# Kernel optimization log

Hardware: AMD Instinct MI355X
Metric: run time of the kernel (lower is better)

## Reference

```python
import jax, jax.numpy as jnp
import numpy as np

NSLICES = 4
HID = 512
IN_DIM = 342   # input_shape - 1 (last column is phase)
OUT_DIM = 311
BATCH = 1024


def _cubic(y0, y1, y2, y3, mu):
    mu2 = mu * mu
    mu3 = mu2 * mu
    return ((-0.5 * y0 + 1.5 * y1 - 1.5 * y2 + 0.5 * y3) * mu3
            + (y0 - 2.5 * y1 + 2.0 * y2 - 0.5 * y3) * mu2
            + (-0.5 * y0 + 0.5 * y2) * mu
            + y1)


def setup_inputs() -> dict:
    key = jax.random.key(0)
    kx, k0, k1, k2 = jax.random.split(key, 4)
    x = jax.random.uniform(kx, (BATCH, IN_DIM + 1), dtype=jnp.float32)
    W0 = jax.random.normal(k0, (NSLICES, HID, IN_DIM), dtype=jnp.float32) * 0.1
    W1 = jax.random.normal(k1, (NSLICES, HID, HID), dtype=jnp.float32) * 0.1
    W2 = jax.random.normal(k2, (NSLICES, OUT_DIM, HID), dtype=jnp.float32) * 0.1
    b0 = jnp.zeros((NSLICES, HID), dtype=jnp.float32)
    b1 = jnp.zeros((NSLICES, HID), dtype=jnp.float32)
    b2 = jnp.zeros((NSLICES, OUT_DIM), dtype=jnp.float32)
    return {"x": x, "W0": W0, "W1": W1, "W2": W2, "b0": b0, "b1": b1, "b2": b2}


def reference(x, W0, W1, W2, b0, b1, b2):
    data, phase = x[:, :-1], x[:, -1]          # [B, 342], [B]
    pscale = NSLICES * phase                    # phase in [0,1) -> pscale in [0,4)
    mu = pscale % 1.0                           # [B]
    i1 = pscale.astype(jnp.int32) % NSLICES
    i0 = (i1 - 1) % NSLICES
    i2 = (i1 + 1) % NSLICES
    i3 = (i1 + 2) % NSLICES

    muW = mu[:, None, None]
    mub = mu[:, None]

    # Per-sample interpolated weights/biases (gather 4 slices + cubic blend)
    W0i = _cubic(W0[i0], W0[i1], W0[i2], W0[i3], muW)   # [B, 512, 342]
    W1i = _cubic(W1[i0], W1[i1], W1[i2], W1[i3], muW)   # [B, 512, 512]
    W2i = _cubic(W2[i0], W2[i1], W2[i2], W2[i3], muW)   # [B, 311, 512]
    b0i = _cubic(b0[i0], b0[i1], b0[i2], b0[i3], mub)   # [B, 512]
    b1i = _cubic(b1[i0], b1[i1], b1[i2], b1[i3], mub)   # [B, 512]
    b2i = _cubic(b2[i0], b2[i1], b2[i2], b2[i3], mub)   # [B, 311]

    # 3-layer MLP with per-sample weights (batched GEMV); dropout in eval mode (identity)
    H1 = jax.nn.elu(jnp.einsum('boi,bi->bo', W0i, data) + b0i)
    H2 = jax.nn.elu(jnp.einsum('boi,bi->bo', W1i, H1) + b1i)
    H3 = jnp.einsum('boi,bi->bo', W2i, H2) + b2i
    return H3
```

## Files before the change

kernel.cpp:

```cpp
#include <hip/hip_runtime.h>
#include <hip/hip_fp16.h>
#include <math.h>

typedef _Float16 f16x8 __attribute__((ext_vector_type(8)));
typedef float f32x4 __attribute__((ext_vector_type(4)));

#define NS 4
#define HID 512
#define IN_DIM 342
#define OUT_DIM 311
#define BATCH 1024
#define INP 352
#define K0V (NS*INP)
#define K12V (NS*HID)
#define XROW (IN_DIM+1)

#define OFF_ACOEF 0
#define OFF_X0H   4096
#define OFF_W0H   (OFF_X0H + 720896)
#define OFF_W1H   (OFF_W0H + 360448)
#define OFF_W2H   (OFF_W1H + 524288)
#define OFF_H1X   (OFF_W2H + 327680)
#define OFF_H2X   OFF_X0H

typedef __attribute__((address_space(3))) void lds_t;
typedef __attribute__((address_space(1))) const void gvm_t;
__device__ __forceinline__ void gload16(const void* g, void* l) {
    __builtin_amdgcn_global_load_lds((gvm_t*)g, (lds_t*)l, 16, 0, 0);
}

__global__ __launch_bounds__(256) void prep_all(
    const float* __restrict__ x,
    const float* __restrict__ W0, const float* __restrict__ W1,
    const float* __restrict__ W2,
    float* __restrict__ acoef,
    __half* __restrict__ X0h, __half* __restrict__ W0h,
    __half* __restrict__ W1h, __half* __restrict__ W2h)
{
    const int bid = blockIdx.x;
    const int t = threadIdx.x;
    if (bid < 512) {
        int o = bid;
        if (t < 176) {
            int s = t / 44;
            int cm = t - s*44;
            int i = cm * 8;
            f16x8 h = {};
            if (i + 8 <= IN_DIM) {
                const float* src = W0 + ((size_t)s*HID + o)*IN_DIM + i;
                float4 v0 = *(const float4*)(src);
                float4 v1 = *(const float4*)(src + 4);
                h[0]=(_Float16)v0.x; h[1]=(_Float16)v0.y; h[2]=(_Float16)v0.z; h[3]=(_Float16)v0.w;
                h[4]=(_Float16)v1.x; h[5]=(_Float16)v1.y; h[6]=(_Float16)v1.z; h[7]=(_Float16)v1.w;
            } else if (i < IN_DIM) {
                const float* src = W0 + ((size_t)s*HID + o)*IN_DIM + i;
                #pragma unroll
                for (int j=0;j<8;++j) h[j] = (_Float16)((i+j < IN_DIM) ? src[j] : 0.f);
            }
            *(f16x8*)(W0h + (size_t)o*K0V + s*INP + i) = h;
        }
    } else if (bid < 1024) {
        int o = bid - 512;
        int k = t * 8;
        int s = k >> 9, i = k & 511;
        const float* src = W1 + ((size_t)s*HID + o)*HID + i;
        float4 v0 = *(const float4*)(src);
        float4 v1 = *(const float4*)(src + 4);
        f16x8 h;
        h[0]=(_Float16)v0.x; h[1]=(_Float16)v0.y; h[2]=(_Float16)v0.z; h[3]=(_Float16)v0.w;
        h[4]=(_Float16)v1.x; h[5]=(_Float16)v1.y; h[6]=(_Float16)v1.z; h[7]=(_Float16)v1.w;
        *(f16x8*)(W1h + (size_t)o*K12V + k) = h;
    } else if (bid < 1344) {
        int o = bid - 1024;
        int k = t * 8;
        int s = k >> 9, i = k & 511;
        f16x8 h = {};
        if (o < OUT_DIM) {
            const float* src = W2 + ((size_t)s*OUT_DIM + o)*HID + i;
            float4 v0 = *(const float4*)(src);
            float4 v1 = *(const float4*)(src + 4);
            h[0]=(_Float16)v0.x; h[1]=(_Float16)v0.y; h[2]=(_Float16)v0.z; h[3]=(_Float16)v0.w;
            h[4]=(_Float16)v1.x; h[5]=(_Float16)v1.y; h[6]=(_Float16)v1.z; h[7]=(_Float16)v1.w;
        }
        *(f16x8*)(W2h + (size_t)o*K12V + k) = h;
    } else {
        int b = bid - 1344;
        float phase = x[(size_t)b*XROW + IN_DIM];
        float ps = (float)NS * phase;
        float mu = ps - floorf(ps);
        int i1 = ((int)ps) & (NS-1);
        float mu2 = mu*mu, mu3 = mu2*mu;
        float r0 =  1.5f*mu3 - 2.5f*mu2 + 1.0f;
        float r1 = -1.5f*mu3 + 2.0f*mu2 + 0.5f*mu;
        float r2 =  0.5f*mu3 - 0.5f*mu2;
        float r3 = -0.5f*mu3 +      mu2 - 0.5f*mu;
        if (t < 4) {
            int rel = (t - i1) & 3;
            acoef[b*4 + t] = (rel==0)?r0:(rel==1)?r1:(rel==2)?r2:r3;
        }
        if (t < 176) {
            int s = t / 44;
            int cm = t - s*44;
            int i = cm * 8;
            int rel = (s - i1) & 3;
            float sc = (rel==0)?r0:(rel==1)?r1:(rel==2)?r2:r3;
            f16x8 h = {};
            if (i + 8 <= IN_DIM) {
                const float* src = x + (size_t)b*XROW + i;
                float4 v0 = *(const float4*)(src);
                float4 v1 = *(const float4*)(src + 4);
                h[0]=(_Float16)(v0.x*sc); h[1]=(_Float16)(v0.y*sc);
                h[2]=(_Float16)(v0.z*sc); h[3]=(_Float16)(v0.w*sc);
                h[4]=(_Float16)(v1.x*sc); h[5]=(_Float16)(v1.y*sc);
                h[6]=(_Float16)(v1.z*sc); h[7]=(_Float16)(v1.w*sc);
            } else if (i < IN_DIM) {
                const float* src = x + (size_t)b*XROW + i;
                #pragma unroll
                for (int j=0;j<8;++j) h[j] = (_Float16)((i+j < IN_DIM) ? src[j]*sc : 0.f);
            }
            *(f16x8*)(X0h + (size_t)b*K0V + s*INP + i) = h;
        }
    }
}

template<int LAYER>
__global__ __launch_bounds__(256) void gemm_mfma(
    const __half* __restrict__ A,
    const __half* __restrict__ Bw,
    const float* __restrict__ acoef,
    const float* __restrict__ bias,
    __half* __restrict__ outH,
    float* __restrict__ outF)
{
    constexpr int K  = (LAYER==0) ? K0V : K12V;
    constexpr int NB = (LAYER==2) ? OUT_DIM : HID;
    constexpr int NITER = K / 128;

    __shared__ __align__(16) char lbuf[4][24576];

    const int t    = threadIdx.x;
    const int lane = t & 63;
    const int wid  = t >> 6;
    const int wm   = wid >> 1;
    const int wn   = wid & 1;
    const int m0   = blockIdx.y * 32;
    const int n0   = blockIdx.x * 64;

    const int cS = lane & 15;
    const int r4 = lane >> 4;
    const int rA0 = 4*(wid    ) + r4;
    const int rA1 = 4*(wid + 4) + r4;
    const __half* aSrc0 = A + (size_t)(m0 + rA0)*K + (((cS&8)|((cS&7)^(rA0&7))) * 8);
    const __half* aSrc1 = A + (size_t)(m0 + rA1)*K + (((cS&8)|((cS&7)^(rA1&7))) * 8);
    const int rB0 = 4*(wid     ) + r4;
    const int rB1 = 4*(wid +  4) + r4;
    const int rB2 = 4*(wid +  8) + r4;
    const int rB3 = 4*(wid + 12) + r4;
    const __half* bSrc0 = Bw + (size_t)(n0 + rB0)*K + (((cS&8)|((cS&7)^(rB0&7))) * 8);
    const __half* bSrc1 = Bw + (size_t)(n0 + rB1)*K + (((cS&8)|((cS&7)^(rB1&7))) * 8);
    const __half* bSrc2 = Bw + (size_t)(n0 + rB2)*K + (((cS&8)|((cS&7)^(rB2&7))) * 8);
    const __half* bSrc3 = Bw + (size_t)(n0 + rB3)*K + (((cS&8)|((cS&7)^(rB3&7))) * 8);

    f32x4 acc[2] = {};

    auto stage = [&](int it) {
        char* base = lbuf[it & 3];
        const int ko = it * 128;
        gload16(aSrc0 + ko, base + (wid    )*1024);
        gload16(aSrc1 + ko, base + (wid + 4)*1024);
        gload16(bSrc0 + ko, base + 8192 + (wid     )*1024);
        gload16(bSrc1 + ko, base + 8192 + (wid +  4)*1024);
        gload16(bSrc2 + ko, base + 8192 + (wid +  8)*1024);
        gload16(bSrc3 + ko, base + 8192 + (wid + 12)*1024);
    };

    stage(0);
    stage(1);
    stage(2);

    for (int it = 0; it < NITER; ++it) {
        if (it + 2 < NITER)      asm volatile("s_waitcnt vmcnt(12)" ::: "memory");
        else if (it + 1 < NITER) asm volatile("s_waitcnt vmcnt(6)"  ::: "memory");
        else                     asm volatile("s_waitcnt vmcnt(0)"  ::: "memory");
        __builtin_amdgcn_s_barrier();
        __builtin_amdgcn_sched_barrier(0);
        if (it + 3 < NITER) stage(it + 3);
        const char* sA = lbuf[it & 3];
        const char* sB = sA + 8192;
        #pragma unroll
        for (int kk = 0; kk < 4; ++kk) {
            const int kb = kk*64 + (lane>>4)*16;
            const int rr = wm*16 + (lane&15);
            f16x8 af = *(const f16x8*)(sA + rr*256 + (kb ^ ((rr&7)<<4)));
            #pragma unroll
            for (int ni = 0; ni < 2; ++ni) {
                const int oo = wn*32 + ni*16 + (lane&15);
                f16x8 bf = *(const f16x8*)(sB + oo*256 + (kb ^ ((oo&7)<<4)));
                acc[ni] = __builtin_amdgcn_mfma_f32_16x16x32_f16(af, bf, acc[ni], 0, 0, 0);
            }
        }
    }

    #pragma unroll
    for (int r = 0; r < 4; ++r) {
        const int row = m0 + wm*16 + (lane>>4)*4 + r;
        const float c0 = acoef[row*4+0], c1 = acoef[row*4+1],
                    c2 = acoef[row*4+2], c3 = acoef[row*4+3];
        #pragma unroll
        for (int ni = 0; ni < 2; ++ni) {
            const int col = n0 + wn*32 + ni*16 + (lane&15);
            float v = acc[ni][r];
            if (LAYER == 2) {
                if (col < OUT_DIM) {
                    float bi = c0*bias[col] + c1*bias[NB+col]
                             + c2*bias[2*NB+col] + c3*bias[3*NB+col];
                    outF[(size_t)row*OUT_DIM + col] = v + bi;
                }
            } else {
                float bi = c0*bias[col] + c1*bias[NB+col]
                         + c2*bias[2*NB+col] + c3*bias[3*NB+col];
                v += bi;
                v = (v > 0.f) ? v : expm1f(v);
                size_t o = (size_t)row*K12V + col;
                outH[o        ] = __float2half(c0*v);
                outH[o +   HID] = __float2half(c1*v);
                outH[o + 2*HID] = __float2half(c2*v);
                outH[o + 3*HID] = __float2half(c3*v);
            }
        }
    }
}

extern "C" void kernel_launch(void* const* d_in, const int* in_sizes, int n_in,
                              void* d_out, int out_size, void* d_ws, size_t ws_size,
                              hipStream_t stream) {
    const float* x  = (const float*)d_in[0];
    const float* W0 = (const float*)d_in[1];
    const float* W1 = (const float*)d_in[2];
    const float* W2 = (const float*)d_in[3];
    const float* b0 = (const float*)d_in[4];
    const float* b1 = (const float*)d_in[5];
    const float* b2 = (const float*)d_in[6];
    float* out = (float*)d_out;
    float* ws  = (float*)d_ws;

    float*  acoef = ws + OFF_ACOEF;
    __half* X0h   = (__half*)(ws + OFF_X0H);
    __half* W0h   = (__half*)(ws + OFF_W0H);
    __half* W1h   = (__half*)(ws + OFF_W1H);
    __half* W2h   = (__half*)(ws + OFF_W2H);
    __half* H1x   = (__half*)(ws + OFF_H1X);
    __half* H2x   = (__half*)(ws + OFF_H2X);

    prep_all<<<dim3(2368), dim3(256), 0, stream>>>(x, W0, W1, W2, acoef,
                                                   X0h, W0h, W1h, W2h);

    gemm_mfma<0><<<dim3(HID/64, BATCH/32), dim3(256), 0, stream>>>(
        X0h, W0h, acoef, b0, H1x, nullptr);
    gemm_mfma<1><<<dim3(HID/64, BATCH/32), dim3(256), 0, stream>>>(
        H1x, W1h, acoef, b1, H2x, nullptr);
    gemm_mfma<2><<<dim3(320/64, BATCH/32), dim3(256), 0, stream>>>(
        H2x, W2h, acoef, b2, nullptr, out);
}
```

Measured before the change: 37.84 us.

## Interleave slice dimension in packed K layout for W1/W2 and hidden activations

Changes the packed fp16 K-dimension layout for layers 1 and 2 from slice-major (s*512+i) to slice-interleaved (i*4+s). The weight packing now reads float2 from all four slices, and the epilogue writes the four coefficient-scaled hidden values as one 8-byte vector store instead of four scattered 2-byte stores. It also loads the four blend coefficients with a single vector load. The aim is cheaper activation stores; the GEMM's K ordering must match consistently between weights and activations, and the weight reads become less contiguous.

Result: no change. 37.74 us (-0.3%).

```diff
diff --git a/kernel.cpp b/kernel.cpp
--- a/kernel.cpp
+++ b/kernel.cpp
@@ -3,6 +3,7 @@
 #include <math.h>
 
 typedef _Float16 f16x8 __attribute__((ext_vector_type(8)));
+typedef _Float16 f16x4 __attribute__((ext_vector_type(4)));
 typedef float f32x4 __attribute__((ext_vector_type(4)));
 
 #define NS 4
@@ -61,28 +62,30 @@
         }
     } else if (bid < 1024) {
         int o = bid - 512;
-        int k = t * 8;
-        int s = k >> 9, i = k & 511;
-        const float* src = W1 + ((size_t)s*HID + o)*HID + i;
-        float4 v0 = *(const float4*)(src);
-        float4 v1 = *(const float4*)(src + 4);
+        int i0 = t * 2;
+        const float* base = W1 + (size_t)o*HID + i0;
+        float2 a0 = *(const float2*)(base + 0*(size_t)HID*HID);
+        float2 a1 = *(const float2*)(base + 1*(size_t)HID*HID);
+        float2 a2 = *(const float2*)(base + 2*(size_t)HID*HID);
+        float2 a3 = *(const float2*)(base + 3*(size_t)HID*HID);
         f16x8 h;
-        h[0]=(_Float16)v0.x; h[1]=(_Float16)v0.y; h[2]=(_Float16)v0.z; h[3]=(_Float16)v0.w;
-        h[4]=(_Float16)v1.x; h[5]=(_Float16)v1.y; h[6]=(_Float16)v1.z; h[7]=(_Float16)v1.w;
-        *(f16x8*)(W1h + (size_t)o*K12V + k) = h;
+        h[0]=(_Float16)a0.x; h[1]=(_Float16)a1.x; h[2]=(_Float16)a2.x; h[3]=(_Float16)a3.x;
+        h[4]=(_Float16)a0.y; h[5]=(_Float16)a1.y; h[6]=(_Float16)a2.y; h[7]=(_Float16)a3.y;
+        *(f16x8*)(W1h + (size_t)o*K12V + t*8) = h;
     } else if (bid < 1344) {
         int o = bid - 1024;
-        int k = t * 8;
-        int s = k >> 9, i = k & 511;
+        int i0 = t * 2;
         f16x8 h = {};
         if (o < OUT_DIM) {
-            const float* src = W2 + ((size_t)s*OUT_DIM + o)*HID + i;
-            float4 v0 = *(const float4*)(src);
-            float4 v1 = *(const float4*)(src + 4);
-            h[0]=(_Float16)v0.x; h[1]=(_Float16)v0.y; h[2]=(_Float16)v0.z; h[3]=(_Float16)v0.w;
-            h[4]=(_Float16)v1.x; h[5]=(_Float16)v1.y; h[6]=(_Float16)v1.z; h[7]=(_Float16)v1.w;
-        }
-        *(f16x8*)(W2h + (size_t)o*K12V + k) = h;
+            const float* base = W2 + (size_t)o*HID + i0;
+            float2 a0 = *(const float2*)(base + 0*(size_t)OUT_DIM*HID);
+            float2 a1 = *(const float2*)(base + 1*(size_t)OUT_DIM*HID);
+            float2 a2 = *(const float2*)(base + 2*(size_t)OUT_DIM*HID);
+            float2 a3 = *(const float2*)(base + 3*(size_t)OUT_DIM*HID);
+            h[0]=(_Float16)a0.x; h[1]=(_Float16)a1.x; h[2]=(_Float16)a2.x; h[3]=(_Float16)a3.x;
+            h[4]=(_Float16)a0.y; h[5]=(_Float16)a1.y; h[6]=(_Float16)a2.y; h[7]=(_Float16)a3.y;
+        }
+        *(f16x8*)(W2h + (size_t)o*K12V + t*8) = h;
     } else {
         int b = bid - 1344;
         float phase = x[(size_t)b*XROW + IN_DIM];
@@ -204,28 +207,26 @@
     #pragma unroll
     for (int r = 0; r < 4; ++r) {
         const int row = m0 + wm*16 + (lane>>4)*4 + r;
-        const float c0 = acoef[row*4+0], c1 = acoef[row*4+1],
-                    c2 = acoef[row*4+2], c3 = acoef[row*4+3];
+        const f32x4 cv = *(const f32x4*)(acoef + row*4);
         #pragma unroll
         for (int ni = 0; ni < 2; ++ni) {
             const int col = n0 + wn*32 + ni*16 + (lane&15);
             float v = acc[ni][r];
             if (LAYER == 2) {
                 if (col < OUT_DIM) {
-                    float bi = c0*bias[col] + c1*bias[NB+col]
-                             + c2*bias[2*NB+col] + c3*bias[3*NB+col];
+                    float bi = cv[0]*bias[col] + cv[1]*bias[NB+col]
+                             + cv[2]*bias[2*NB+col] + cv[3]*bias[3*NB+col];
                     outF[(size_t)row*OUT_DIM + col] = v + bi;
                 }
             } else {
-                float bi = c0*bias[col] + c1*bias[NB+col]
-                         + c2*bias[2*NB+col] + c3*bias[3*NB+col];
+                float bi = cv[0]*bias[col] + cv[1]*bias[NB+col]
+                         + cv[2]*bias[2*NB+col] + cv[3]*bias[3*NB+col];
                 v += bi;
                 v = (v > 0.f) ? v : expm1f(v);
-                size_t o = (size_t)row*K12V + col;
-                outH[o        ] = __float2half(c0*v);
-                outH[o +   HID] = __float2half(c1*v);
-                outH[o + 2*HID] = __float2half(c2*v);
-                outH[o + 3*HID] = __float2half(c3*v);
+                f16x4 hv;
+                hv[0]=(_Float16)(cv[0]*v); hv[1]=(_Float16)(cv[1]*v);
+                hv[2]=(_Float16)(cv[2]*v); hv[3]=(_Float16)(cv[3]*v);
+                *(f16x4*)(outH + (size_t)row*K12V + col*4) = hv;
             }
         }
     }
```
